# Kernel optimization log

Measured on AMD Instinct MI355X. Metric: run time of the kernel, lower is better.

The kernel has to match this reference:

```python
import jax, jax.numpy as jnp
from jax import lax
import numpy as np

N, C, H, W = 8, 32, 64, 64
KS, NB = 7, 6            # kernel_size, num_bases
TB = (KS // 2) * NB      # total_bases = 18
BC = TB * NB             # bc_dim = 108
INTER = max(64, BC // 2) # 64
OUT = 64
PAD = KS // 2
EPS = 1e-5


def conv3x3(x, w, b):
    # x: (N,Cin,H,W), w: (Cout,Cin,3,3)
    y = lax.conv_general_dilated(x, w, (1, 1), [(1, 1), (1, 1)],
                                 dimension_numbers=('NCHW', 'OIHW', 'NCHW'))
    return y + b[None, :, None, None]


def batchnorm(x, g, b):
    # training-mode BN: batch stats over (N,H,W)
    mu = jnp.mean(x, axis=(0, 2, 3), keepdims=True)
    var = jnp.var(x, axis=(0, 2, 3), keepdims=True)
    return (x - mu) * lax.rsqrt(var + EPS) * g[None, :, None, None] + b[None, :, None, None]


def setup_inputs() -> dict:
    key = jax.random.key(0)
    ks = jax.random.split(key, 12)
    s = 0.05
    # random bases as in get_random_bases: (TB, KS*KS), zero-mean-ish rows
    f = jax.random.normal(ks[0], (TB, KS * KS), dtype=jnp.float32)
    bases = f - jnp.mean(f, axis=1, keepdims=True) / jnp.std(f, axis=1, keepdims=True)
    return {
        'x': jax.random.normal(ks[1], (N, C, H, W), dtype=jnp.float32),
        'conv1_w': jax.random.normal(ks[2], (INTER, C, 3, 3), dtype=jnp.float32) * s,
        'conv1_b': jax.random.normal(ks[3], (INTER,), dtype=jnp.float32) * s,
        'bn1_g': jnp.ones((INTER,), jnp.float32),
        'bn1_b': jnp.zeros((INTER,), jnp.float32),
        'conv2_w': jax.random.normal(ks[4], (BC, INTER, 3, 3), dtype=jnp.float32) * s,
        'conv2_b': jax.random.normal(ks[5], (BC,), dtype=jnp.float32) * s,
        'bn2_g': jnp.ones((BC,), jnp.float32),
        'bn2_b': jnp.zeros((BC,), jnp.float32),
        'bases': bases,
        'out_w': jax.random.normal(ks[6], (OUT, C * NB), dtype=jnp.float32) * s,
        'out_b': jax.random.normal(ks[7], (OUT,), dtype=jnp.float32) * s,
    }


def reference(x, conv1_w, conv1_b, bn1_g, bn1_b, conv2_w, conv2_b,
              bn2_g, bn2_b, bases, out_w, out_b):
    # bases_net: conv3x3 -> BN -> tanh -> conv3x3 -> BN -> tanh
    h = jnp.tanh(batchnorm(conv3x3(x, conv1_w, conv1_b), bn1_g, bn1_b))
    coef = jnp.tanh(batchnorm(conv3x3(h, conv2_w, conv2_b), bn2_g, bn2_b))
    # (N, BC, H, W) -> (N, NB, TB, H, W) -> (N, H, W, NB, TB)
    coef = coef.reshape(N, NB, TB, H, W).transpose(0, 3, 4, 1, 2)
    # atoms: (coef[...,None] * bases).sum(-2).transpose(-1,-2) => (N,H,W,KS^2,NB)
    atoms = jnp.einsum('nhwmt,tk->nhwkm', coef, bases)
    # unfold: channel-major (C, ks, ks) flattened, matching F.unfold
    patches = lax.conv_general_dilated_patches(
        x, (KS, KS), (1, 1), [(PAD, PAD), (PAD, PAD)],
        dimension_numbers=('NCHW', 'OIHW', 'NCHW'))  # (N, C*KS*KS, H, W)
    patches = patches.reshape(N, C, KS * KS, H, W)
    # per-pixel contraction over ks^2: (N,H,W,C,NB)
    bases_out = jnp.einsum('nckhw,nhwkm->nhwcm', patches, atoms)
    bases_out = bases_out.reshape(N, H, W, C * NB)
    out = jnp.einsum('nhwd,od->nohw', bases_out, out_w) + out_b[None, :, None, None]
    return out
```

## Files before the change

kernel.cpp:

```cpp
#include <hip/hip_runtime.h>
#include <hip/hip_bf16.h>

#define N_ 8
#define C_ 32
#define H_ 64
#define W_ 64
#define HW_ (H_*W_)
#define NHW_ (N_*HW_)
#define INTER_ 64
#define BC_ 108
#define KS_ 7
#define K2_ (KS_*KS_)
#define NB_ 6
#define TB_ 18
#define OUT_ 64
#define DDIM_ (C_*NB_)
#define P2CH_ 288

typedef __attribute__((ext_vector_type(8))) short short8;
typedef __attribute__((ext_vector_type(4))) float f32x4;
typedef __attribute__((ext_vector_type(2))) float f32x2;

__device__ __forceinline__ unsigned short f2bf(float f) {
    union { float f; unsigned u; } v; v.f = f;
    unsigned r = v.u + 0x7fffu + ((v.u >> 16) & 1u);
    return (unsigned short)(r >> 16);
}
__device__ __forceinline__ float bf2f(unsigned short h) {
    return __uint_as_float((unsigned int)h << 16);
}

__device__ __forceinline__ short8 frag4(const unsigned int* p) {
    union { unsigned int u[4]; short8 s; } v;
    v.u[0] = p[0]; v.u[1] = p[1]; v.u[2] = p[2]; v.u[3] = p[3];
    return v.s;
}

template<int TP0, int NTP>
__device__ __forceinline__ void pconv_pass(const float (*sx)[44],
                                           const float* __restrict__ bases,
                                           unsigned int* __restrict__ P2,
                                           int n, int c, int r0, int rb, int lane) {
    f32x2 av[NTP][4];
    #pragma unroll
    for (int tp = 0; tp < NTP; tp++)
        #pragma unroll
        for (int rr = 0; rr < 4; rr++) av[tp][rr] = (f32x2){0.f, 0.f};

    #pragma unroll 1
    for (int kx = 0; kx < 7; kx++) {
        float rw[12];
        const float* sp = &sx[lane + kx][rb];
        #pragma unroll
        for (int qq = 0; qq < 3; qq++) {
            float4 r4 = *(const float4*)(sp + qq * 4);
            rw[qq * 4 + 0] = r4.x; rw[qq * 4 + 1] = r4.y;
            rw[qq * 4 + 2] = r4.z; rw[qq * 4 + 3] = r4.w;
        }
        #pragma unroll
        for (int tp = 0; tp < NTP; tp++) {
            #pragma unroll
            for (int ky = 0; ky < 7; ky++) {
                f32x2 w2;
                w2.x = bases[(2 * (TP0 + tp)) * K2_ + ky * 7 + kx];
                w2.y = bases[(2 * (TP0 + tp) + 1) * K2_ + ky * 7 + kx];
                #pragma unroll
                for (int rr = 0; rr < 4; rr++) {
                    float xv = rw[rr + ky];
                    f32x2 xv2 = (f32x2){xv, xv};
                    av[tp][rr] += xv2 * w2;
                }
            }
        }
    }

    #pragma unroll
    for (int tp = 0; tp < NTP; tp++)
        #pragma unroll
        for (int rr = 0; rr < 4; rr++) {
            int gr = r0 + rb + rr;
            unsigned int pk = (unsigned int)f2bf(av[tp][rr].x) |
                              ((unsigned int)f2bf(av[tp][rr].y) << 16);
            P2[(((size_t)n * P2CH_ + (TP0 + tp) * 32 + c) << 12) + (gr << 6) + lane] = pk;
        }
}

__global__ __launch_bounds__(256) void k_front(const float* __restrict__ x,
                                               const float* __restrict__ bases,
                                               const float* __restrict__ w1,
                                               const float* __restrict__ w2,
                                               const float* __restrict__ ow,
                                               unsigned short* __restrict__ xb,
                                               unsigned short* __restrict__ wb1,
                                               unsigned short* __restrict__ wb2,
                                               unsigned short* __restrict__ wbp,
                                               unsigned int* __restrict__ P2,
                                               float* __restrict__ pz) {
    __shared__ __align__(16) char smem[70 * 44 * 4];
    int bid = blockIdx.x, t = threadIdx.x;

    if (bid < 1024) {
        float (*sx)[44] = (float(*)[44])smem;
        int rq = bid & 3;
        int c  = (bid >> 2) & 31;
        int n  = bid >> 7;
        int lane = t & 63, wv = t >> 6;
        int r0 = rq << 4;

        const float* xc = x + (((size_t)n * C_ + c) << 12);
        #pragma unroll
        for (int j = 0; j < 6; j++) {
            int p = wv + 4 * j;
            if (p < 22) {
                int grow = r0 - 3 + p;
                bool rowok = (grow >= 0 && grow < H_);
                int wx = lane - 3;
                float v = 0.f;
                if (rowok && wx >= 0) v = xc[(grow << 6) + wx];
                sx[lane][p] = v;
                if (lane < 6) {
                    int wx2 = 61 + lane;
                    float v2 = 0.f;
                    if (rowok && wx2 < W_) v2 = xc[(grow << 6) + wx2];
                    sx[64 + lane][p] = v2;
                }
            }
        }
        __syncthreads();

        int rb = wv * 4;
        pconv_pass<0, 5>(sx, bases, P2, n, c, r0, rb, lane);
        pconv_pass<5, 4>(sx, bases, P2, n, c, r0, rb, lane);
    } else {
        int pbid = bid - 1024;
        if (pbid < 512) {
            unsigned short* sT = (unsigned short*)smem;
            int n = pbid >> 6, hw0 = (pbid << 6) & 4095;
            for (int i = t; i < 2048; i += 256) {
                int c = i >> 6, px = i & 63;
                float v = x[(((size_t)n * C_ + c) << 12) + hw0 + px];
                sT[px * 36 + c] = f2bf(v);
            }
            __syncthreads();
            unsigned int* xd = (unsigned int*)xb;
            for (int i = t; i < 1024; i += 256) {
                int px = i >> 4, cw = i & 15;
                unsigned int lo = sT[px * 36 + cw * 2], hi = sT[px * 36 + cw * 2 + 1];
                xd[(((size_t)n << 12) + hw0 + px) * 16 + cw] = lo | (hi << 16);
            }
        } else if (pbid < 584) {
            int i = (pbid - 512) * 256 + t;
            int ci = i & 31, co = (i >> 5) & 63, s = i >> 11;
            wb1[i] = f2bf(w1[((co << 5) + ci) * 9 + s]);
        } else if (pbid < 872) {
            int i = (pbid - 584) * 256 + t;
            int ci = i & 63, co = (i >> 6) & 127, s = i >> 13;
            unsigned short v = 0;
            if (co < BC_) v = f2bf(w2[((co << 6) + ci) * 9 + s]);
            wb2[i] = v;
        } else if (pbid < 920) {
            int i = (pbid - 872) * 256 + t;
            if (i < OUT_ * DDIM_) {
                float v = ow[i];
                unsigned short hi = f2bf(v);
                wbp[i] = hi;
                wbp[OUT_ * DDIM_ + i] = f2bf(v - bf2f(hi));
            }
        } else {
            for (int i = t; i < (INTER_ + BC_) * 8 * 2; i += 256) pz[i] = 0.f;
        }
    }
}

template<int CIN, int COG, int ROWS, int WPAD, int NCOQ>
__global__ __launch_bounds__(256) void k_conv3(const unsigned short* __restrict__ xb,
                                               const unsigned short* __restrict__ wb,
                                               const float* __restrict__ bias,
                                               float* __restrict__ y,
                                               float2* __restrict__ part,
                                               int COUT_real) {
    constexpr int CPAD = CIN + 8;
    constexpr int NSLC = (ROWS + 2) * 66;
    constexpr int MT = COG / 16;
    constexpr int NTW = ROWS;
    constexpr int KSTEPS = CIN / 32;
    __shared__ unsigned short sx[NSLC * CPAD];
    __shared__ unsigned short sw[9 * COG * CPAD];
    __shared__ float sbp[4][COG * 2];

    int bid = blockIdx.x;
    int coq = bid % NCOQ;
    int rp = (bid / NCOQ) % (H_ / ROWS);
    int n = bid / (NCOQ * (H_ / ROWS));
    int h0 = rp * ROWS;
    int co0 = coq * COG;
    int t = threadIdx.x;
    int lane = t & 63, wv = t >> 6;
    int q = lane >> 4, n15 = lane & 15;

    {
        const unsigned int* xg = (const unsigned int*)xb + (size_t)n * HW_ * (CIN / 2);
        unsigned int* sxd = (unsigned int*)sx;
        constexpr int DW = CIN / 2;
        constexpr int DWPT = DW / 8;
        int part_ = t & 7;
        for (int sl = (t >> 3); sl < NSLC; sl += 32) {
            int r = sl / 66, col = sl % 66;
            int hh = h0 - 1 + r, ww = col - 1;
            unsigned int v[DWPT];
            #pragma unroll
            for (int i = 0; i < DWPT; i++) v[i] = 0;
            if (hh >= 0 && hh < H_ && ww >= 0 && ww < W_) {
                const unsigned int* gp = xg + (size_t)(hh * W_ + ww) * DW + part_ * DWPT;
                #pragma unroll
                for (int i = 0; i < DWPT; i++) v[i] = gp[i];
            }
            unsigned int* d = sxd + sl * (CPAD / 2) + part_ * DWPT;
            #pragma unroll
            for (int i = 0; i < DWPT; i++) d[i] = v[i];
        }
    }
    {
        const unsigned int* wg = (const unsigned int*)wb;
        unsigned int* swd = (unsigned int*)sw;
        constexpr int TOT = 9 * COG * (CIN / 2);
        for (int e = t; e < TOT; e += 256) {
            int s_co = e / (CIN / 2), cw = e % (CIN / 2);
            int s = s_co / COG, co = s_co % COG;
            swd[s_co * (CPAD / 2) + cw] = wg[((size_t)s * WPAD + co0 + co) * (CIN / 2) + cw];
        }
    }
    __syncthreads();

    f32x4 acc[NTW][MT];
    #pragma unroll
    for (int a = 0; a < NTW; a++)
        #pragma unroll
        for (int m = 0; m < MT; m++) acc[a][m] = (f32x4){0.f, 0.f, 0.f, 0.f};

    #pragma unroll
    for (int s = 0; s < 9; s++) {
        int dy = s / 3, dx = s % 3;
        #pragma unroll
        for (int kc = 0; kc < KSTEPS; kc++) {
            int ci0 = kc * 32;
            short8 bfr[NTW];
            #pragma unroll
            for (int ntl = 0; ntl < NTW; ntl++) {
                int nt = wv * NTW + ntl;
                int r_out = nt >> 2, col0 = (nt & 3) * 16;
                bfr[ntl] = *(const short8*)(sx + ((r_out + dy) * 66 + col0 + n15 + dx) * CPAD + ci0 + q * 8);
            }
            #pragma unroll
            for (int mt = 0; mt < MT; mt++) {
                short8 afr = *(const short8*)(sw + ((s * COG) + mt * 16 + n15) * CPAD + ci0 + q * 8);
                #pragma unroll
                for (int ntl = 0; ntl < NTW; ntl++)
                    acc[ntl][mt] = __builtin_amdgcn_mfma_f32_16x16x32_bf16(afr, bfr[ntl], acc[ntl][mt], 0, 0, 0);
            }
        }
    }

    float sacc[MT][4], sacc2[MT][4];
    #pragma unroll
    for (int mt = 0; mt < MT; mt++)
        #pragma unroll
        for (int reg = 0; reg < 4; reg++) { sacc[mt][reg] = 0.f; sacc2[mt][reg] = 0.f; }

    #pragma unroll
    for (int ntl = 0; ntl < NTW; ntl++) {
        int nt = wv * NTW + ntl;
        int h = h0 + (nt >> 2), wcol = (nt & 3) * 16 + n15;
        #pragma unroll
        for (int mt = 0; mt < MT; mt++) {
            #pragma unroll
            for (int reg = 0; reg < 4; reg++) {
                int co = co0 + mt * 16 + q * 4 + reg;
                if (co < COUT_real) {
                    float v = acc[ntl][mt][reg] + bias[co];
                    y[(((size_t)n * COUT_real + co) << 12) + h * W_ + wcol] = v;
                    sacc[mt][reg] += v;
                    sacc2[mt][reg] += v * v;
                }
            }
        }
    }

    #pragma unroll
    for (int mt = 0; mt < MT; mt++)
        #pragma unroll
        for (int reg = 0; reg < 4; reg++) {
            float s = sacc[mt][reg], s2 = sacc2[mt][reg];
            #pragma unroll
            for (int off = 1; off < 16; off <<= 1) {
                s += __shfl_xor(s, off);
                s2 += __shfl_xor(s2, off);
            }
            if (n15 == 0) {
                int cl = mt * 16 + q * 4 + reg;
                sbp[wv][cl * 2] = s;
                sbp[wv][cl * 2 + 1] = s2;
            }
        }
    __syncthreads();
    if (t < COG) {
        float s = 0.f, s2 = 0.f;
        #pragma unroll
        for (int w2 = 0; w2 < 4; w2++) { s += sbp[w2][t * 2]; s2 += sbp[w2][t * 2 + 1]; }
        int co = co0 + t;
        if (co < COUT_real) {
            atomicAdd(&part[(co << 3) + n].x, s);
            atomicAdd(&part[(co << 3) + n].y, s2);
        }
    }
}

__global__ __launch_bounds__(256) void k_bntr(const float* __restrict__ y1,
                                              const float2* __restrict__ part,
                                              const float* __restrict__ g,
                                              const float* __restrict__ bb,
                                              unsigned short* __restrict__ y1b) {
    __shared__ unsigned short sT[64 * 68];
    __shared__ float scs[INTER_], shs[INTER_];
    int bid = blockIdx.x, t = threadIdx.x;
    int n = bid >> 6, hw0 = (bid << 6) & 4095;
    if (t < INTER_) {
        float s = 0.f, s2 = 0.f;
        #pragma unroll
        for (int j = 0; j < 8; j++) { float2 p = part[t * 8 + j]; s += p.x; s2 += p.y; }
        float mu = s / (float)NHW_, var = s2 / (float)NHW_ - mu * mu;
        float sc = g[t] * rsqrtf(var + 1e-5f);
        scs[t] = sc; shs[t] = bb[t] - mu * sc;
    }
    __syncthreads();
    for (int i = t; i < 4096; i += 256) {
        int c = i >> 6, px = i & 63;
        float v = y1[(((size_t)n * INTER_ + c) << 12) + hw0 + px];
        sT[px * 68 + c] = f2bf(tanhf(v * scs[c] + shs[c]));
    }
    __syncthreads();
    unsigned int* yd = (unsigned int*)y1b;
    for (int i = t; i < 2048; i += 256) {
        int px = i >> 5, cw = i & 31;
        unsigned int lo = sT[px * 68 + cw * 2], hi = sT[px * 68 + cw * 2 + 1];
        yd[(((size_t)n << 12) + hw0 + px) * 32 + cw] = lo | (hi << 16);
    }
}

#define YPAD_ 97
__global__ __launch_bounds__(256) void k_ytail(const float* __restrict__ y2,
                                               const float2* __restrict__ part,
                                               const float* __restrict__ g,
                                               const float* __restrict__ bb,
                                               const unsigned int* __restrict__ P2,
                                               const unsigned short* __restrict__ wbp,
                                               const float* __restrict__ out_b,
                                               float* __restrict__ out) {
    __shared__ float scs[BC_], shs[BC_];
    __shared__ float cfs[BC_][32];
    __shared__ unsigned int sYh[32 * YPAD_];
    __shared__ unsigned int sYl[32 * YPAD_];

    int bid = blockIdx.x;
    int n = bid >> 7, px0 = (bid & 127) << 5;
    int t = threadIdx.x;

    int px = t & 31, cg = t >> 5;
    unsigned int u[4][9];
    {
        const unsigned int* Pb = P2 + (((size_t)n * P2CH_) << 12) + px0 + px;
        #pragma unroll
        for (int cc = 0; cc < 4; cc++) {
            int c = cg * 4 + cc;
            #pragma unroll
            for (int tp = 0; tp < 9; tp++)
                u[cc][tp] = Pb[(size_t)(tp * 32 + c) << 12];
        }
    }

    if (t < BC_) {
        float s = 0.f, s2 = 0.f;
        #pragma unroll
        for (int j = 0; j < 8; j++) { float2 p = part[t * 8 + j]; s += p.x; s2 += p.y; }
        float mu = s / (float)NHW_, var = s2 / (float)NHW_ - mu * mu;
        float sc = g[t] * rsqrtf(var + 1e-5f);
        scs[t] = sc; shs[t] = bb[t] - mu * sc;
    }
    __syncthreads();

    for (int i = t; i < BC_ * 32; i += 256) {
        int ch = i >> 5, pxx = i & 31;
        float v = y2[(((size_t)n * BC_ + ch) << 12) + px0 + pxx];
        cfs[ch][pxx] = tanhf(v * scs[ch] + shs[ch]);
    }
    __syncthreads();

    {
        f32x2 pv2[2][TB_];
        #pragma unroll
        for (int j = 0; j < 2; j++)
            #pragma unroll
            for (int tp = 0; tp < 9; tp++) {
                pv2[j][2 * tp].x     = __uint_as_float(u[2 * j][tp] << 16);
                pv2[j][2 * tp].y     = __uint_as_float(u[2 * j + 1][tp] << 16);
                pv2[j][2 * tp + 1].x = __uint_as_float(u[2 * j][tp] & 0xffff0000u);
                pv2[j][2 * tp + 1].y = __uint_as_float(u[2 * j + 1][tp] & 0xffff0000u);
            }
        f32x2 ym2[2][NB_];
        #pragma unroll
        for (int j = 0; j < 2; j++)
            #pragma unroll
            for (int m = 0; m < NB_; m++) ym2[j][m] = (f32x2){0.f, 0.f};
        #pragma unroll
        for (int m = 0; m < NB_; m++)
            #pragma unroll
            for (int tt = 0; tt < TB_; tt++) {
                float cfv = cfs[m * TB_ + tt][px];
                f32x2 c2 = (f32x2){cfv, cfv};
                ym2[0][m] += c2 * pv2[0][tt];
                ym2[1][m] += c2 * pv2[1][tt];
            }
        #pragma unroll
        for (int j = 0; j < 2; j++) {
            #pragma unroll
            for (int half = 0; half < 2; half++) {
                int c = cg * 4 + 2 * j + half;
                #pragma unroll
                for (int jj = 0; jj < 3; jj++) {
                    float y0 = half ? ym2[j][2 * jj].y     : ym2[j][2 * jj].x;
                    float y1v = half ? ym2[j][2 * jj + 1].y : ym2[j][2 * jj + 1].x;
                    unsigned short h0 = f2bf(y0);
                    unsigned short h1 = f2bf(y1v);
                    unsigned short l0 = f2bf(y0 - bf2f(h0));
                    unsigned short l1 = f2bf(y1v - bf2f(h1));
                    sYh[px * YPAD_ + c * 3 + jj] = (unsigned int)h0 | ((unsigned int)h1 << 16);
                    sYl[px * YPAD_ + c * 3 + jj] = (unsigned int)l0 | ((unsigned int)l1 << 16);
                }
            }
        }
    }
    __syncthreads();

    int lane = t & 63, wv = t >> 6;
    int q = lane >> 4, n15 = lane & 15;
    f32x4 acc[2];
    acc[0] = (f32x4){0.f, 0.f, 0.f, 0.f};
    acc[1] = (f32x4){0.f, 0.f, 0.f, 0.f};
    #pragma unroll
    for (int ks = 0; ks < 6; ks++) {
        short8 ah = *(const short8*)(wbp + (wv * 16 + n15) * DDIM_ + ks * 32 + q * 8);
        short8 al = *(const short8*)(wbp + OUT_ * DDIM_ + (wv * 16 + n15) * DDIM_ + ks * 32 + q * 8);
        #pragma unroll
        for (int nt = 0; nt < 2; nt++) {
            short8 bh = frag4(sYh + (nt * 16 + n15) * YPAD_ + ks * 16 + q * 4);
            short8 bl = frag4(sYl + (nt * 16 + n15) * YPAD_ + ks * 16 + q * 4);
            acc[nt] = __builtin_amdgcn_mfma_f32_16x16x32_bf16(ah, bh, acc[nt], 0, 0, 0);
            acc[nt] = __builtin_amdgcn_mfma_f32_16x16x32_bf16(ah, bl, acc[nt], 0, 0, 0);
            acc[nt] = __builtin_amdgcn_mfma_f32_16x16x32_bf16(al, bh, acc[nt], 0, 0, 0);
        }
    }
    #pragma unroll
    for (int nt = 0; nt < 2; nt++)
        #pragma unroll
        for (int reg = 0; reg < 4; reg++) {
            int o = wv * 16 + q * 4 + reg;
            out[(((size_t)n * OUT_ + o) << 12) + px0 + nt * 16 + n15] = acc[nt][reg] + out_b[o];
        }
}

extern "C" void kernel_launch(void* const* d_in, const int* in_sizes, int n_in,
                              void* d_out, int out_size, void* d_ws, size_t ws_size,
                              hipStream_t stream) {
    const float* x       = (const float*)d_in[0];
    const float* conv1_w = (const float*)d_in[1];
    const float* conv1_b = (const float*)d_in[2];
    const float* bn1_g   = (const float*)d_in[3];
    const float* bn1_b   = (const float*)d_in[4];
    const float* conv2_w = (const float*)d_in[5];
    const float* conv2_b = (const float*)d_in[6];
    const float* bn2_g   = (const float*)d_in[7];
    const float* bn2_b   = (const float*)d_in[8];
    const float* bases   = (const float*)d_in[9];
    const float* out_w   = (const float*)d_in[10];
    const float* out_b   = (const float*)d_in[11];
    float* out = (float*)d_out;

    float* y1  = (float*)d_ws;
    float* y2  = y1 + (size_t)N_ * INTER_ * HW_;
    unsigned int* P2 = (unsigned int*)(y2 + (size_t)N_ * BC_ * HW_);
    unsigned short* xb  = (unsigned short*)(P2 + (size_t)N_ * P2CH_ * HW_);
    unsigned short* y1b = xb + (size_t)NHW_ * C_;
    unsigned short* wb1 = y1b + (size_t)NHW_ * INTER_;
    unsigned short* wb2 = wb1 + 9 * 64 * 32;
    unsigned short* wbp = wb2 + 9 * 128 * 64;
    float2* part1 = (float2*)(wbp + 2 * OUT_ * DDIM_);
    float2* part2 = part1 + INTER_ * 8;

    k_front<<<1945, 256, 0, stream>>>(x, bases, conv1_w, conv2_w, out_w,
                                      xb, wb1, wb2, wbp, P2, (float*)part1);

    k_conv3<C_, 64, 1, 64, 1><<<N_ * 64, 256, 0, stream>>>(
        xb, wb1, conv1_b, y1, part1, INTER_);
    k_bntr<<<512, 256, 0, stream>>>(y1, part1, bn1_g, bn1_b, y1b);

    k_conv3<INTER_, 16, 2, 128, 7><<<N_ * 32 * 7, 256, 0, stream>>>(
        y1b, wb2, conv2_b, y2, part2, BC_);

    k_ytail<<<1024, 256, 0, stream>>>(y2, (const float2*)part2, bn2_g, bn2_b,
                                      P2, wbp, out_b, out);
}
```

Measured before the change: 207.5 us.

## Fuse conv1 into front kernel, reading fp32 x directly and dropping the x transpose

The conv1 3x3 convolution and its batch-norm partial statistics now run inside the front kernel as extra blocks. Each block loads fp32 x rows and converts them to a bf16 halo tile in shared memory, converts its conv1 weight slice, and runs MFMA. This removes the separate bf16 x-transpose pass, the wb1 preparation and one kernel launch. The stats buffer zeroing moves to a hipMemsetAsync. In exchange, each conv1 block reloads three input rows and redoes the weight conversion, the row loads use only 96 threads with a serial column loop, and statistics are merged with atomics.

```diff
diff --git a/kernel.cpp b/kernel.cpp
--- a/kernel.cpp
+++ b/kernel.cpp
@@ -90,13 +90,13 @@
                                                const float* __restrict__ w1,
                                                const float* __restrict__ w2,
                                                const float* __restrict__ ow,
-                                               unsigned short* __restrict__ xb,
-                                               unsigned short* __restrict__ wb1,
+                                               const float* __restrict__ b1,
                                                unsigned short* __restrict__ wb2,
                                                unsigned short* __restrict__ wbp,
                                                unsigned int* __restrict__ P2,
-                                               float* __restrict__ pz) {
-    __shared__ __align__(16) char smem[70 * 44 * 4];
+                                               float* __restrict__ y1,
+                                               float2* __restrict__ part1) {
+    __shared__ __align__(16) char smem[39936];
     int bid = blockIdx.x, t = threadIdx.x;
 
     if (bid < 1024) {
@@ -131,43 +131,103 @@
         int rb = wv * 4;
         pconv_pass<0, 5>(sx, bases, P2, n, c, r0, rb, lane);
         pconv_pass<5, 4>(sx, bases, P2, n, c, r0, rb, lane);
+    } else if (bid < 2048) {
+        unsigned short* sx1 = (unsigned short*)smem;
+        unsigned short* sw1 = sx1 + 198 * 40;
+        float* sbp = (float*)(sw1 + 9 * 32 * 40);
+
+        int cid = bid - 1024;
+        int n = cid >> 7;
+        int rem = cid & 127;
+        int co0 = (rem & 1) << 5;
+        int h0 = rem >> 1;
+        int lane = t & 63, wv = t >> 6;
+        int q = lane >> 4, n15 = lane & 15;
+
+        if (t < 96) {
+            int c = t & 31, r = t >> 5;
+            int hh = h0 - 1 + r;
+            bool rok = (hh >= 0 && hh < H_);
+            const float* xr = x + (((size_t)n * C_ + c) << 12) + (hh << 6);
+            sx1[(r * 66 + 0) * 40 + c] = 0;
+            sx1[(r * 66 + 65) * 40 + c] = 0;
+            #pragma unroll 4
+            for (int col = 1; col <= 64; col++) {
+                float v = rok ? xr[col - 1] : 0.f;
+                sx1[(r * 66 + col) * 40 + c] = f2bf(v);
+            }
+        }
+        for (int e = t; e < 9 * 32 * 32; e += 256) {
+            int ci = e & 31, co = (e >> 5) & 31, s = e >> 10;
+            sw1[(s * 32 + co) * 40 + ci] = f2bf(w1[(((co0 + co) << 5) + ci) * 9 + s]);
+        }
+        __syncthreads();
+
+        f32x4 acc[2];
+        acc[0] = (f32x4){0.f, 0.f, 0.f, 0.f};
+        acc[1] = (f32x4){0.f, 0.f, 0.f, 0.f};
+        #pragma unroll
+        for (int s = 0; s < 9; s++) {
+            int dy = s / 3, dx = s % 3;
+            short8 bfr = *(const short8*)(sx1 + (dy * 66 + wv * 16 + n15 + dx) * 40 + q * 8);
+            #pragma unroll
+            for (int mt = 0; mt < 2; mt++) {
+                short8 afr = *(const short8*)(sw1 + (s * 32 + mt * 16 + n15) * 40 + q * 8);
+                acc[mt] = __builtin_amdgcn_mfma_f32_16x16x32_bf16(afr, bfr, acc[mt], 0, 0, 0);
+            }
+        }
+
+        int wcol = wv * 16 + n15;
+        float sa[2][4], sa2[2][4];
+        #pragma unroll
+        for (int mt = 0; mt < 2; mt++)
+            #pragma unroll
+            for (int reg = 0; reg < 4; reg++) {
+                int co = co0 + mt * 16 + q * 4 + reg;
+                float v = acc[mt][reg] + b1[co];
+                y1[(((size_t)n * INTER_ + co) << 12) + (h0 << 6) + wcol] = v;
+                sa[mt][reg] = v; sa2[mt][reg] = v * v;
+            }
+        #pragma unroll
+        for (int mt = 0; mt < 2; mt++)
+            #pragma unroll
+            for (int reg = 0; reg < 4; reg++) {
+                float s = sa[mt][reg], s2 = sa2[mt][reg];
+                #pragma unroll
+                for (int off = 1; off < 16; off <<= 1) {
+                    s += __shfl_xor(s, off);
+                    s2 += __shfl_xor(s2, off);
+                }
+                if (n15 == 0) {
+                    int cl = mt * 16 + q * 4 + reg;
+                    sbp[wv * 64 + cl * 2] = s;
+                    sbp[wv * 64 + cl * 2 + 1] = s2;
+                }
+            }
+        __syncthreads();
+        if (t < 32) {
+            float s = 0.f, s2 = 0.f;
+            #pragma unroll
+            for (int w = 0; w < 4; w++) { s += sbp[w * 64 + t * 2]; s2 += sbp[w * 64 + t * 2 + 1]; }
+            atomicAdd(&part1[((co0 + t) << 3) + n].x, s);
+            atomicAdd(&part1[((co0 + t) << 3) + n].y, s2);
+        }
     } else {
-        int pbid = bid - 1024;
-        if (pbid < 512) {
-            unsigned short* sT = (unsigned short*)smem;
-            int n = pbid >> 6, hw0 = (pbid << 6) & 4095;
-            for (int i = t; i < 2048; i += 256) {
-                int c = i >> 6, px = i & 63;
-                float v = x[(((size_t)n * C_ + c) << 12) + hw0 + px];
-                sT[px * 36 + c] = f2bf(v);
-            }
-            __syncthreads();
-            unsigned int* xd = (unsigned int*)xb;
-            for (int i = t; i < 1024; i += 256) {
-                int px = i >> 4, cw = i & 15;
-                unsigned int lo = sT[px * 36 + cw * 2], hi = sT[px * 36 + cw * 2 + 1];
-                xd[(((size_t)n << 12) + hw0 + px) * 16 + cw] = lo | (hi << 16);
-            }
-        } else if (pbid < 584) {
-            int i = (pbid - 512) * 256 + t;
-            int ci = i & 31, co = (i >> 5) & 63, s = i >> 11;
-            wb1[i] = f2bf(w1[((co << 5) + ci) * 9 + s]);
-        } else if (pbid < 872) {
-            int i = (pbid - 584) * 256 + t;
+        int pbid = bid - 2048;
+        if (pbid < 288) {
+            int i = pbid * 256 + t;
             int ci = i & 63, co = (i >> 6) & 127, s = i >> 13;
             unsigned short v = 0;
             if (co < BC_) v = f2bf(w2[((co << 6) + ci) * 9 + s]);
             wb2[i] = v;
-        } else if (pbid < 920) {
-            int i = (pbid - 872) * 256 + t;
+        } else {
+            int i = (pbid - 288) * 256 + t;
             if (i < OUT_ * DDIM_) {
                 float v = ow[i];
                 unsigned short hi = f2bf(v);
                 wbp[i] = hi;
                 wbp[OUT_ * DDIM_ + i] = f2bf(v - bf2f(hi));
             }
-        } else {
-            for (int i = t; i < (INTER_ + BC_) * 8 * 2; i += 256) pz[i] = 0.f;
         }
     }
 }
@@ -496,11 +556,11 @@
     float2* part1 = (float2*)(wbp + 2 * OUT_ * DDIM_);
     float2* part2 = part1 + INTER_ * 8;
 
-    k_front<<<1945, 256, 0, stream>>>(x, bases, conv1_w, conv2_w, out_w,
-                                      xb, wb1, wb2, wbp, P2, (float*)part1);
-
-    k_conv3<C_, 64, 1, 64, 1><<<N_ * 64, 256, 0, stream>>>(
-        xb, wb1, conv1_b, y1, part1, INTER_);
+    hipMemsetAsync(part1, 0, (size_t)(INTER_ + BC_) * 8 * sizeof(float2), stream);
+
+    k_front<<<2384, 256, 0, stream>>>(x, bases, conv1_w, conv2_w, out_w, conv1_b,
+                                      wb2, wbp, P2, y1, part1);
+
     k_bntr<<<512, 256, 0, stream>>>(y1, part1, bn1_g, bn1_b, y1b);
 
     k_conv3<INTER_, 16, 2, 128, 7><<<N_ * 32 * 7, 256, 0, stream>>>(
```

After: 216.6 us. +4.3%, slower.
